# Kernel tuning notes

Hardware: AMD Instinct MI355X
Metric: run time of the kernel (lower is better)

## Reference

```python
import jax, jax.numpy as jnp
import numpy as np


def setup_inputs() -> dict:
    key = jax.random.key(0)
    k1, k2, k3, k4 = jax.random.split(key, 4)
    B, S, H, P = 8, 2048, 1024, 4096
    hidden_states = jax.random.normal(k1, (B, S, H), dtype=jnp.float32)
    pairs = jax.random.randint(k2, (B, P, 2), 0, S, dtype=jnp.int64)
    # classifier params: Linear(2H -> H), Linear(H -> 2). Stored as (in, out).
    W1 = jax.random.normal(k3, (2 * H, H), dtype=jnp.float32) * (1.0 / np.sqrt(2 * H))
    b1 = jnp.zeros((H,), dtype=jnp.float32)
    W2 = jax.random.normal(k4, (H, 2), dtype=jnp.float32) * (1.0 / np.sqrt(H))
    b2 = jnp.zeros((2,), dtype=jnp.float32)
    return {"hidden_states": hidden_states, "pairs": pairs,
            "W1": W1, "b1": b1, "W2": W2, "b2": b2}


def reference(hidden_states, pairs, W1, b1, W2, b2):
    # Gather pair embeddings: (B, P, H) each.
    emb1 = jnp.take_along_axis(hidden_states, pairs[:, :, 0:1], axis=1)
    emb2 = jnp.take_along_axis(hidden_states, pairs[:, :, 1:2], axis=1)
    pair_emb = jnp.concatenate([emb1, emb2], axis=-1)  # (B, P, 2H)
    h = jnp.einsum('bpi,ih->bph', pair_emb, W1) + b1
    h = jax.nn.gelu(h, approximate=False)  # torch nn.GELU default is exact erf
    # Dropout is identity at inference.
    logits = jnp.einsum('bph,ho->bpo', h, W2) + b2  # (B, P, 2)
    return logits
```

## Files before the change

kernel.cpp:

```cpp
#include <hip/hip_runtime.h>
#include <hip/hip_bf16.h>

#define B_  8
#define S_  2048
#define H_  1024
#define P_  4096
#define K_  2048
#define M_  32768
#define NKT 64

typedef unsigned short u16;
using bf16x8 = __attribute__((ext_vector_type(8))) short;
using f32x4  = __attribute__((ext_vector_type(4))) float;

#define AS1 __attribute__((address_space(1)))
#define AS3 __attribute__((address_space(3)))

__device__ inline u16 f2bf(float f) {
  union { float f; unsigned u; } c; c.f = f;
  unsigned u = c.u;
  unsigned r = (u + 0x7fffu + ((u >> 16) & 1u)) >> 16;
  return (u16)r;
}

__global__ void cvt_hidden_k(const float4* __restrict__ src,
                             ushort4* __restrict__ dst, int n4) {
  int i = blockIdx.x * blockDim.x + threadIdx.x;
  int stride = gridDim.x * blockDim.x;
  for (; i < n4; i += stride) {
    float4 v = src[i];
    ushort4 o;
    o.x = f2bf(v.x); o.y = f2bf(v.y); o.z = f2bf(v.z); o.w = f2bf(v.w);
    dst[i] = o;
  }
}

__global__ void transp_w1_k(const float* __restrict__ w1, u16* __restrict__ w1t) {
  __shared__ float tile[32][33];
  int n0 = blockIdx.x * 32;
  int k0 = blockIdx.y * 32;
  int tx = threadIdx.x;
  int ty = threadIdx.y;
#pragma unroll
  for (int i = 0; i < 32; i += 8)
    tile[ty + i][tx] = w1[(size_t)(k0 + ty + i) * H_ + n0 + tx];
  __syncthreads();
#pragma unroll
  for (int i = 0; i < 32; i += 8)
    w1t[(size_t)(n0 + ty + i) * K_ + k0 + tx] = f2bf(tile[tx][ty + i]);
}

__global__ __launch_bounds__(512, 2) void gemm_k(
    const u16*  __restrict__ hidB,
    const u16*  __restrict__ w1t,
    const int*  __restrict__ pairs,
    const float* __restrict__ b1,
    const float2* __restrict__ w2,
    float*      __restrict__ part)
{
  __shared__ u16 ldsA[4][256 * 32];
  __shared__ u16 ldsB[4][256 * 32];

  int orig = blockIdx.x;
  int bid = (orig & 7) * (512 >> 3) + (orig >> 3);
  int nt = bid & 3;
  int mt = bid >> 2;
  int n0 = nt * 256;
  int m0 = mt * 256;
  int bI = m0 >> 12;
  int pp = m0 & 4095;

  int t = threadIdx.x;
  int w = t >> 6;
  int l = t & 63;
  int lr = l & 15;
  int lj = l >> 4;
  int wr = w >> 2;
  int wn = w & 3;

  int r0 = w * 16 + (l >> 2);
  int r1 = 128 + r0;
  int g0 = (l & 3) ^ (r0 & 3);

  int2 sv0 = ((const int2*)pairs)[bI * P_ + pp + r0];
  int2 sv1 = ((const int2*)pairs)[bI * P_ + pp + r1];

  const u16* hidBase = hidB + ((size_t)bI << 21);

  f32x4 acc[8][4];
#pragma unroll
  for (int i = 0; i < 8; ++i)
#pragma unroll
    for (int j = 0; j < 4; ++j)
      acc[i][j] = (f32x4){0.f, 0.f, 0.f, 0.f};

  auto STAGE = [&](int buf, int kt) {
    int k0 = kt * 32;
    int kcol = k0 & 1023;
    int half = k0 >> 10;
    int sA0 = half ? sv0.y : sv0.x;
    int sA1 = half ? sv1.y : sv1.x;
    __builtin_amdgcn_global_load_lds(
        (const AS1 void*)(hidBase + (((size_t)sA0) << 10) + kcol + g0 * 8),
        (AS3 void*)&ldsA[buf][w * 512 + l * 8], 16, 0, 0);
    __builtin_amdgcn_global_load_lds(
        (const AS1 void*)(hidBase + (((size_t)sA1) << 10) + kcol + g0 * 8),
        (AS3 void*)&ldsA[buf][4096 + w * 512 + l * 8], 16, 0, 0);
    __builtin_amdgcn_global_load_lds(
        (const AS1 void*)(w1t + (size_t)(n0 + r0) * K_ + k0 + g0 * 8),
        (AS3 void*)&ldsB[buf][w * 512 + l * 8], 16, 0, 0);
    __builtin_amdgcn_global_load_lds(
        (const AS1 void*)(w1t + (size_t)(n0 + r1) * K_ + k0 + g0 * 8),
        (AS3 void*)&ldsB[buf][4096 + w * 512 + l * 8], 16, 0, 0);
  };

#define PHASE(KT, DOSTAGE, WAITOP)                                            \
  {                                                                           \
    const int buf_ = (KT) & 3;                                                \
    bf16x8 af[8], bv[4];                                                      \
    _Pragma("unroll")                                                         \
    for (int mi = 0; mi < 8; ++mi) {                                          \
      int row = wr * 128 + mi * 16 + lr;                                      \
      af[mi] = *(const bf16x8*)&ldsA[buf_][row * 32 + ((lj ^ (row & 3)) * 8)];\
    }                                                                         \
    _Pragma("unroll")                                                         \
    for (int ni = 0; ni < 4; ++ni) {                                          \
      int row = wn * 64 + ni * 16 + lr;                                       \
      bv[ni] = *(const bf16x8*)&ldsB[buf_][row * 32 + ((lj ^ (row & 3)) * 8)];\
    }                                                                         \
    if (DOSTAGE) STAGE((KT + 3) & 3, (KT) + 3);                               \
    WAITOP;                                                                   \
    __builtin_amdgcn_s_barrier();                                             \
    __builtin_amdgcn_s_setprio(1);                                            \
    _Pragma("unroll")                                                         \
    for (int mi = 0; mi < 8; ++mi)                                            \
      _Pragma("unroll")                                                       \
      for (int ni = 0; ni < 4; ++ni)                                          \
        acc[mi][ni] = __builtin_amdgcn_mfma_f32_16x16x32_bf16(                \
            af[mi], bv[ni], acc[mi][ni], 0, 0, 0);                            \
    __builtin_amdgcn_s_setprio(0);                                            \
    __builtin_amdgcn_s_barrier();                                             \
    asm volatile("" ::: "memory");                                            \
  }

  STAGE(0, 0); STAGE(1, 1); STAGE(2, 2);
  asm volatile("s_waitcnt vmcnt(8)" ::: "memory");
  __builtin_amdgcn_s_barrier();

  for (int kt = 0; kt < NKT - 3; ++kt)
    PHASE(kt, true, asm volatile("s_waitcnt vmcnt(8)" ::: "memory"));
  PHASE(NKT - 3, false, asm volatile("s_waitcnt vmcnt(4)" ::: "memory"));
  PHASE(NKT - 2, false, asm volatile("s_waitcnt vmcnt(0)" ::: "memory"));
  PHASE(NKT - 1, false, );
#undef PHASE

  int q = nt * 4 + wn;
  float2* pOut = (float2*)part;
#pragma unroll
  for (int mi = 0; mi < 8; ++mi) {
    float s0[4] = {0.f, 0.f, 0.f, 0.f};
    float s1[4] = {0.f, 0.f, 0.f, 0.f};
#pragma unroll
    for (int ni = 0; ni < 4; ++ni) {
      int n = n0 + wn * 64 + ni * 16 + lr;
      float bb = b1[n];
      float2 wv = w2[n];
#pragma unroll
      for (int j = 0; j < 4; ++j) {
        float x = acc[mi][ni][j] + bb;
        float g = 0.5f * x * (1.0f + erff(x * 0.70710678118654752f));
        s0[j] += g * wv.x;
        s1[j] += g * wv.y;
      }
    }
#pragma unroll
    for (int off = 1; off < 16; off <<= 1) {
#pragma unroll
      for (int j = 0; j < 4; ++j) {
        s0[j] += __shfl_xor(s0[j], off, 64);
        s1[j] += __shfl_xor(s1[j], off, 64);
      }
    }
    if (lr == 0) {
#pragma unroll
      for (int j = 0; j < 4; ++j) {
        int m = m0 + wr * 128 + mi * 16 + lj * 4 + j;
        pOut[((size_t)q << 15) + m] = make_float2(s0[j], s1[j]);
      }
    }
  }
}

__global__ void reduce_k(const float2* __restrict__ part,
                         const float* __restrict__ b2,
                         float2* __restrict__ out) {
  int m = blockIdx.x * blockDim.x + threadIdx.x;
  if (m >= M_) return;
  float a0 = b2[0], a1 = b2[1];
#pragma unroll
  for (int q = 0; q < 16; ++q) {
    float2 v = part[((size_t)q << 15) + m];
    a0 += v.x; a1 += v.y;
  }
  out[m] = make_float2(a0, a1);
}

extern "C" void kernel_launch(void* const* d_in, const int* in_sizes, int n_in,
                              void* d_out, int out_size, void* d_ws, size_t ws_size,
                              hipStream_t stream) {
  const float* hidden = (const float*)d_in[0];
  const int*   pairs  = (const int*)d_in[1];
  const float* W1     = (const float*)d_in[2];
  const float* b1     = (const float*)d_in[3];
  const float* W2     = (const float*)d_in[4];
  const float* b2     = (const float*)d_in[5];
  float* out = (float*)d_out;

  u16* hidB = (u16*)d_ws;
  u16* w1t  = hidB + (size_t)B_ * S_ * H_;
  float* part = (float*)(w1t + (size_t)H_ * K_);

  int n4 = (B_ * S_ * H_) / 4;
  cvt_hidden_k<<<4096, 256, 0, stream>>>((const float4*)hidden, (ushort4*)hidB, n4);
  transp_w1_k<<<dim3(H_ / 32, K_ / 32), dim3(32, 8), 0, stream>>>(W1, w1t);
  gemm_k<<<(M_ / 256) * (H_ / 256), 512, 0, stream>>>(
      hidB, w1t, pairs, b1, (const float2*)W2, part);
  reduce_k<<<(M_ + 255) / 256, 256, 0, stream>>>(
      (const float2*)part, b2, (float2*)out);
}
```

Before: 189.2 us.

## Split each k-step into two M-half phases with finer-grained staggered staging

Restructures the GEMM main loop so each 32-wide k-slice is processed in two phases, each doing half the M fragments, with A and B global-to-LDS loads issued in separate phases. It uses a single flat LDS buffer of four regions over two 64-wide k tiles, and changes the LDS swizzle to depend on the lane index. The aim is to interleave memory issue with MFMA work more finely, cut register pressure from A fragments, and shorten waits between barriers. In exchange there are twice as many barriers per k-slice, explicit lgkmcnt waits and sched barriers, and a more complex wait-count schedule that could stall if mistuned.

```diff
diff --git a/kernel.cpp b/kernel.cpp
--- a/kernel.cpp
+++ b/kernel.cpp
@@ -7,7 +7,6 @@
 #define P_  4096
 #define K_  2048
 #define M_  32768
-#define NKT 64
 
 typedef unsigned short u16;
 using bf16x8 = __attribute__((ext_vector_type(8))) short;
@@ -58,11 +57,12 @@
     const float2* __restrict__ w2,
     float*      __restrict__ part)
 {
-  __shared__ u16 ldsA[4][256 * 32];
-  __shared__ u16 ldsB[4][256 * 32];
+  __shared__ u16 lds[65536];
+
+#define REG(SLOT, KS, AB) ((((SLOT)*2 + (KS))*2 + (AB)) * 8192)
 
   int orig = blockIdx.x;
-  int bid = (orig & 7) * (512 >> 3) + (orig >> 3);
+  int bid = (orig & 7) * 64 + (orig >> 3);
   int nt = bid & 3;
   int mt = bid >> 2;
   int n0 = nt * 256;
@@ -78,9 +78,11 @@
   int wr = w >> 2;
   int wn = w & 3;
 
+  int slot8 = (lj ^ ((l >> 1) & 3)) * 8;
+  int gsrc = (l & 3) ^ ((l >> 3) & 3);
+
   int r0 = w * 16 + (l >> 2);
   int r1 = 128 + r0;
-  int g0 = (l & 3) ^ (r0 & 3);
 
   int2 sv0 = ((const int2*)pairs)[bI * P_ + pp + r0];
   int2 sv1 = ((const int2*)pairs)[bI * P_ + pp + r1];
@@ -94,64 +96,91 @@
     for (int j = 0; j < 4; ++j)
       acc[i][j] = (f32x4){0.f, 0.f, 0.f, 0.f};
 
-  auto STAGE = [&](int buf, int kt) {
-    int k0 = kt * 32;
-    int kcol = k0 & 1023;
-    int half = k0 >> 10;
+  auto STAGE_A = [&](int base, int tile, int ks) {
+    int k = tile * 64 + ks * 32;
+    int kcol = k & 1023;
+    int half = k >> 10;
     int sA0 = half ? sv0.y : sv0.x;
     int sA1 = half ? sv1.y : sv1.x;
-    __builtin_amdgcn_global_load_lds(
-        (const AS1 void*)(hidBase + (((size_t)sA0) << 10) + kcol + g0 * 8),
-        (AS3 void*)&ldsA[buf][w * 512 + l * 8], 16, 0, 0);
-    __builtin_amdgcn_global_load_lds(
-        (const AS1 void*)(hidBase + (((size_t)sA1) << 10) + kcol + g0 * 8),
-        (AS3 void*)&ldsA[buf][4096 + w * 512 + l * 8], 16, 0, 0);
-    __builtin_amdgcn_global_load_lds(
-        (const AS1 void*)(w1t + (size_t)(n0 + r0) * K_ + k0 + g0 * 8),
-        (AS3 void*)&ldsB[buf][w * 512 + l * 8], 16, 0, 0);
-    __builtin_amdgcn_global_load_lds(
-        (const AS1 void*)(w1t + (size_t)(n0 + r1) * K_ + k0 + g0 * 8),
-        (AS3 void*)&ldsB[buf][4096 + w * 512 + l * 8], 16, 0, 0);
+    int dst = base + w * 512 + l * 8;
+    __builtin_amdgcn_global_load_lds(
+        (const AS1 void*)(hidBase + (((size_t)sA0) << 10) + kcol + gsrc * 8),
+        (AS3 void*)&lds[dst], 16, 0, 0);
+    __builtin_amdgcn_global_load_lds(
+        (const AS1 void*)(hidBase + (((size_t)sA1) << 10) + kcol + gsrc * 8),
+        (AS3 void*)&lds[dst + 4096], 16, 0, 0);
   };
-
-#define PHASE(KT, DOSTAGE, WAITOP)                                            \
-  {                                                                           \
-    const int buf_ = (KT) & 3;                                                \
-    bf16x8 af[8], bv[4];                                                      \
-    _Pragma("unroll")                                                         \
-    for (int mi = 0; mi < 8; ++mi) {                                          \
-      int row = wr * 128 + mi * 16 + lr;                                      \
-      af[mi] = *(const bf16x8*)&ldsA[buf_][row * 32 + ((lj ^ (row & 3)) * 8)];\
-    }                                                                         \
-    _Pragma("unroll")                                                         \
-    for (int ni = 0; ni < 4; ++ni) {                                          \
-      int row = wn * 64 + ni * 16 + lr;                                       \
-      bv[ni] = *(const bf16x8*)&ldsB[buf_][row * 32 + ((lj ^ (row & 3)) * 8)];\
-    }                                                                         \
-    if (DOSTAGE) STAGE((KT + 3) & 3, (KT) + 3);                               \
-    WAITOP;                                                                   \
-    __builtin_amdgcn_s_barrier();                                             \
-    __builtin_amdgcn_s_setprio(1);                                            \
-    _Pragma("unroll")                                                         \
-    for (int mi = 0; mi < 8; ++mi)                                            \
-      _Pragma("unroll")                                                       \
-      for (int ni = 0; ni < 4; ++ni)                                          \
-        acc[mi][ni] = __builtin_amdgcn_mfma_f32_16x16x32_bf16(                \
-            af[mi], bv[ni], acc[mi][ni], 0, 0, 0);                            \
-    __builtin_amdgcn_s_setprio(0);                                            \
-    __builtin_amdgcn_s_barrier();                                             \
-    asm volatile("" ::: "memory");                                            \
-  }
-
-  STAGE(0, 0); STAGE(1, 1); STAGE(2, 2);
+  auto STAGE_B = [&](int base, int tile, int ks) {
+    int k = tile * 64 + ks * 32;
+    int dst = base + w * 512 + l * 8;
+    __builtin_amdgcn_global_load_lds(
+        (const AS1 void*)(w1t + (size_t)(n0 + r0) * K_ + k + gsrc * 8),
+        (AS3 void*)&lds[dst], 16, 0, 0);
+    __builtin_amdgcn_global_load_lds(
+        (const AS1 void*)(w1t + (size_t)(n0 + r1) * K_ + k + gsrc * 8),
+        (AS3 void*)&lds[dst + 4096], 16, 0, 0);
+  };
+
+#define VM6 asm volatile("s_waitcnt vmcnt(6)" ::: "memory")
+#define VM4 asm volatile("s_waitcnt vmcnt(4)" ::: "memory")
+#define VM0 asm volatile("s_waitcnt vmcnt(0)" ::: "memory")
+
+  bf16x8 bv[4];
+
+#define PHASE(SLOT, KS, MH, STAGEOP, WAITOP)                                   \
+  {                                                                            \
+    bf16x8 af[4];                                                              \
+    _Pragma("unroll")                                                          \
+    for (int mi = 0; mi < 4; ++mi)                                             \
+      af[mi] = *(const bf16x8*)&lds[REG(SLOT, KS, 0) +                         \
+          (wr * 128 + (MH) * 64 + mi * 16 + lr) * 32 + slot8];                 \
+    if ((MH) == 0) {                                                           \
+      _Pragma("unroll")                                                        \
+      for (int ni = 0; ni < 4; ++ni)                                           \
+        bv[ni] = *(const bf16x8*)&lds[REG(SLOT, KS, 1) +                       \
+            (wn * 64 + ni * 16 + lr) * 32 + slot8];                            \
+    }                                                                          \
+    STAGEOP;                                                                   \
+    WAITOP;                                                                    \
+    __builtin_amdgcn_s_barrier();                                              \
+    asm volatile("s_waitcnt lgkmcnt(0)" ::: "memory");                         \
+    __builtin_amdgcn_sched_barrier(0);                                         \
+    __builtin_amdgcn_s_setprio(1);                                             \
+    _Pragma("unroll")                                                          \
+    for (int mi = 0; mi < 4; ++mi)                                             \
+      _Pragma("unroll")                                                        \
+      for (int ni = 0; ni < 4; ++ni)                                           \
+        acc[(MH) * 4 + mi][ni] = __builtin_amdgcn_mfma_f32_16x16x32_bf16(      \
+            af[mi], bv[ni], acc[(MH) * 4 + mi][ni], 0, 0, 0);                  \
+    __builtin_amdgcn_s_setprio(0);                                             \
+    __builtin_amdgcn_s_barrier();                                              \
+  }
+
+  STAGE_A(REG(0, 0, 0), 0, 0); STAGE_B(REG(0, 0, 1), 0, 0);
+  STAGE_A(REG(0, 1, 0), 0, 1); STAGE_B(REG(0, 1, 1), 0, 1);
+  STAGE_A(REG(1, 0, 0), 1, 0); STAGE_B(REG(1, 0, 1), 1, 0);
   asm volatile("s_waitcnt vmcnt(8)" ::: "memory");
   __builtin_amdgcn_s_barrier();
 
-  for (int kt = 0; kt < NKT - 3; ++kt)
-    PHASE(kt, true, asm volatile("s_waitcnt vmcnt(8)" ::: "memory"));
-  PHASE(NKT - 3, false, asm volatile("s_waitcnt vmcnt(4)" ::: "memory"));
-  PHASE(NKT - 2, false, asm volatile("s_waitcnt vmcnt(0)" ::: "memory"));
-  PHASE(NKT - 1, false, );
+  for (int u = 0; u < 15; ++u) {
+    int t1 = 2 * u + 1, t2 = 2 * u + 2, t3 = 2 * u + 3;
+    PHASE(0, 0, 0, STAGE_A(REG(1, 1, 0), t1, 1), VM6);
+    PHASE(0, 0, 1, STAGE_B(REG(1, 1, 1), t1, 1), );
+    PHASE(0, 1, 0, STAGE_A(REG(0, 0, 0), t2, 0), VM6);
+    PHASE(0, 1, 1, STAGE_B(REG(0, 0, 1), t2, 0), );
+    PHASE(1, 0, 0, STAGE_A(REG(0, 1, 0), t2, 1), VM6);
+    PHASE(1, 0, 1, STAGE_B(REG(0, 1, 1), t2, 1), );
+    PHASE(1, 1, 0, STAGE_A(REG(1, 0, 0), t3, 0), VM6);
+    PHASE(1, 1, 1, STAGE_B(REG(1, 0, 1), t3, 0), );
+  }
+  PHASE(0, 0, 0, STAGE_A(REG(1, 1, 0), 31, 1), VM6);
+  PHASE(0, 0, 1, STAGE_B(REG(1, 1, 1), 31, 1), );
+  PHASE(0, 1, 0, , VM4);
+  PHASE(0, 1, 1, , );
+  PHASE(1, 0, 0, , VM0);
+  PHASE(1, 0, 1, , );
+  PHASE(1, 1, 0, , );
+  PHASE(1, 1, 1, , );
 #undef PHASE
 
   int q = nt * 4 + wn;
```

New measurement: 173.3 us. -8.4%, faster.
